# Performance work log

Measured on AMD Instinct MI355X. Metric: run time of the kernel, lower is better.

Reference implementation:

```python
import jax, jax.numpy as jnp
import numpy as np

B, C, F = 4, 3, 5
HO, WO = 256, 256
HI, WI = HO + F - 1, WO + F - 1


def setup_inputs() -> dict:
    key = jax.random.key(0)
    k = jax.random.split(key, 6)
    return {
        "tensorInput": jax.random.normal(k[0], (B, C, HI, WI), dtype=jnp.float32),
        "tensorVertical": jax.random.uniform(k[1], (B, F, HO, WO), dtype=jnp.float32),
        "tensorHorizontal": jax.random.uniform(k[2], (B, F, HO, WO), dtype=jnp.float32),
        "tensorOffsetX": jax.random.normal(k[3], (B, F * F, HO, WO), dtype=jnp.float32),
        "tensorOffsetY": jax.random.normal(k[4], (B, F * F, HO, WO), dtype=jnp.float32),
        "tensorMask": jax.random.uniform(k[5], (B, F * F, HO, WO), dtype=jnp.float32),
    }


def _dsepconv(inp, vertical, horizontal, offset_x, offset_y, mask):
    b, c, hin, win = inp.shape
    f = vertical.shape[1]
    ho, wo = vertical.shape[2], vertical.shape[3]
    half = (f - 1) / 2.0

    fy = jnp.arange(f, dtype=inp.dtype).reshape(f, 1, 1, 1)
    fx = jnp.arange(f, dtype=inp.dtype).reshape(1, f, 1, 1)
    hg = jnp.arange(ho, dtype=inp.dtype).reshape(1, 1, ho, 1)
    wg = jnp.arange(wo, dtype=inp.dtype).reshape(1, 1, 1, wo)

    off_y = offset_y.reshape(b, f, f, ho, wo)  # note: code uses offset_y for delta_x
    off_x = offset_x.reshape(b, f, f, ho, wo)  # and offset_x for delta_y

    # sample positions per tap, [B,F,F,Ho,Wo]
    px = jnp.clip(off_y + wg + fx - half + 1.0, 0.0, win - 1)
    py = jnp.clip(off_x + hg + fy - half + 1.0, 0.0, hin - 1)

    left_f = jnp.floor(px)
    top_f = jnp.floor(py)
    wx = 1.0 - (px - left_f)  # bilinear weights
    wy = 1.0 - (py - top_f)

    l = left_f.astype(jnp.int32)
    t = top_f.astype(jnp.int32)
    r = jnp.minimum(l + 1, win - 1)
    btm = jnp.minimum(t + 1, hin - 1)

    def gather(img, yi, xi):
        return img[:, yi, xi]

    g = jax.vmap(gather)
    v_tl = g(inp, t, l)
    v_tr = g(inp, t, r)
    v_bl = g(inp, btm, l)
    v_br = g(inp, btm, r)

    wx_ = wx[:, None]  # add channel axis -> [B,1,F,F,Ho,Wo]
    wy_ = wy[:, None]
    val = (v_tl * wx_ * wy_ + v_tr * (1 - wx_) * wy_
           + v_bl * wx_ * (1 - wy_) + v_br * (1 - wx_) * (1 - wy_))

    # separable filter x mask per tap: [B,F,F,Ho,Wo]
    w_tap = vertical[:, :, None] * horizontal[:, None, :] * mask.reshape(b, f, f, ho, wo)
    # accumulate over the F*F taps
    return jnp.sum(val * w_tap[:, None], axis=(2, 3))  # [B,C,Ho,Wo]


def reference(tensorInput, tensorVertical, tensorHorizontal, tensorOffsetX, tensorOffsetY, tensorMask):
    return _dsepconv(tensorInput, tensorVertical, tensorHorizontal,
                     tensorOffsetX, tensorOffsetY, tensorMask)
```

## Files before the change

kernel.cpp:

```cpp
#include <hip/hip_runtime.h>
#include <hip/hip_fp16.h>

constexpr int B  = 4;
constexpr int C  = 3;
constexpr int F  = 5;
constexpr int HO = 256;
constexpr int WO = 256;
constexpr int HI = HO + F - 1;
constexpr int WI = WO + F - 1;
constexpr int P  = HO * WO;
constexpr int FF = F * F;
constexpr int PI = HI * WI;

constexpr int TROWS = 18;
constexpr int TCOLS = 80;
constexpr int TSTRIDE = 81;
constexpr int TN = TROWS * TCOLS;
constexpr int AMAX = (TROWS - 2) * TSTRIDE + (TCOLS - 2);

__device__ __forceinline__ uint2 pack3(float a, float b, float c) {
    __half2 ab = __floats2half2_rn(a, b);
    __half2 cz = __floats2half2_rn(c, 0.0f);
    uint2 r;
    r.x = *reinterpret_cast<const unsigned int*>(&ab);
    r.y = *reinterpret_cast<const unsigned int*>(&cz);
    return r;
}

__device__ __forceinline__ void fmacc(uint2 v, float w,
                                      float& a0, float& a1, float& a2) {
    __half2 ab = *reinterpret_cast<const __half2*>(&v.x);
    __half2 cz = *reinterpret_cast<const __half2*>(&v.y);
    a0 += __half2float(__low2half(ab))  * w;
    a1 += __half2float(__high2half(ab)) * w;
    a2 += __half2float(__low2half(cz))  * w;
}

__global__ __launch_bounds__(320, 8) void dsepconv_kernel(
    const float* __restrict__ inp,
    const float* __restrict__ vert,
    const float* __restrict__ horz,
    const float* __restrict__ offX,
    const float* __restrict__ offY,
    const float* __restrict__ mask,
    float* __restrict__ out)
{
    __shared__ uint2 tileq[TROWS * TSTRIDE];

    const int tid  = threadIdx.x;
    const int lane = tid & 63;
    const int wave = tid >> 6;

    const int idx0 = blockIdx.x * 64;
    const int idx  = idx0 + lane;
    const int x    = idx & (WO - 1);
    const int y    = (idx >> 8) & (HO - 1);
    const int b    = idx >> 16;
    const int x0   = idx0 & (WO - 1);
    const int pix  = y * WO + x;

    const float* in0 = inp + (size_t)b * C * PI;
    const float* in1 = in0 + PI;
    const float* in2 = in1 + PI;

    const int ry0 = y - 7;
    const int cx0 = x0 - 7;
#pragma unroll 1
    for (int e = tid; e < TN; e += 320) {
        int trow = e / TCOLS;
        int tcol = e - trow * TCOLS;
        int gy = min(max(ry0 + trow, 0), HI - 1);
        int gx = min(max(cx0 + tcol, 0), WI - 1);
        int g = gy * WI + gx;
        tileq[trow * TSTRIDE + tcol] = pack3(in0[g], in1[g], in2[g]);
    }
    __syncthreads();

    const float* offXb = offX + (size_t)b * FF * P + pix;
    const float* offYb = offY + (size_t)b * FF * P + pix;
    const float* maskb = mask + (size_t)b * FF * P + pix;
    const float* vb    = vert + (size_t)b * F * P + pix;
    const float* hb    = horz + (size_t)b * F * P + pix;

    const int i = wave;
    const float v = vb[i * P];
    const float py_base = (float)(y + i - 1);

    float acc0 = 0.f, acc1 = 0.f, acc2 = 0.f;

#pragma unroll 1
    for (int j = 0; j < F; ++j) {
        const int k = i * F + j;

        float oy = offYb[k * P];
        float ox = offXb[k * P];
        float m  = maskb[k * P];
        float h  = hb[j * P];

        float px = fminf(fmaxf(oy + (float)(x + j - 1), 0.0f), (float)(WI - 1));
        float py = fminf(fmaxf(ox + py_base, 0.0f), (float)(HI - 1));

        float lf = floorf(px);
        float tf = floorf(py);
        int l = (int)lf;
        int t = (int)tf;
        float wx = 1.0f - (px - lf);
        float wy = 1.0f - (py - tf);

        float w   = v * h * m;
        float wyw = wy * w;
        float wbw = w - wyw;
        float wtl = wx * wyw;
        float wtr = wyw - wtl;
        float wbl = wx * wbw;
        float wbr = wbw - wbl;

        int lt = t - ry0;
        int ll = l - cx0;
        bool ok = ((unsigned)lt <= TROWS - 2) & ((unsigned)ll <= TCOLS - 2);

        int a = min(max(lt * TSTRIDE + ll, 0), AMAX);

        uint2 g_tl = tileq[a];
        uint2 g_tr = tileq[a + 1];
        uint2 g_bl = tileq[a + TSTRIDE];
        uint2 g_br = tileq[a + TSTRIDE + 1];

        if (__any(!ok)) {
            if (!ok) {
                int r  = min(l + 1, WI - 1);
                int bt = min(t + 1, HI - 1);
                int o_tl = t * WI + l,  o_tr = t * WI + r;
                int o_bl = bt * WI + l, o_br = bt * WI + r;
                g_tl = pack3(in0[o_tl], in1[o_tl], in2[o_tl]);
                g_tr = pack3(in0[o_tr], in1[o_tr], in2[o_tr]);
                g_bl = pack3(in0[o_bl], in1[o_bl], in2[o_bl]);
                g_br = pack3(in0[o_br], in1[o_br], in2[o_br]);
            }
        }

        fmacc(g_tl, wtl, acc0, acc1, acc2);
        fmacc(g_tr, wtr, acc0, acc1, acc2);
        fmacc(g_bl, wbl, acc0, acc1, acc2);
        fmacc(g_br, wbr, acc0, acc1, acc2);
    }

    __syncthreads();
    float* red = (float*)tileq;
    red[(wave * 3 + 0) * 64 + lane] = acc0;
    red[(wave * 3 + 1) * 64 + lane] = acc1;
    red[(wave * 3 + 2) * 64 + lane] = acc2;
    __syncthreads();

    if (tid < 192) {
        const int ch = tid >> 6;
        const int ln = tid & 63;
        float s = red[(0 * 3 + ch) * 64 + ln]
                + red[(1 * 3 + ch) * 64 + ln]
                + red[(2 * 3 + ch) * 64 + ln]
                + red[(3 * 3 + ch) * 64 + ln]
                + red[(4 * 3 + ch) * 64 + ln];
        const int sidx = idx0 + ln;
        const int sb   = sidx >> 16;
        const int spix = sidx & (P - 1);
        out[(size_t)sb * C * P + (size_t)ch * P + spix] = s;
    }
}

extern "C" void kernel_launch(void* const* d_in, const int* in_sizes, int n_in,
                              void* d_out, int out_size, void* d_ws, size_t ws_size,
                              hipStream_t stream) {
    const float* inp  = (const float*)d_in[0];
    const float* vert = (const float*)d_in[1];
    const float* horz = (const float*)d_in[2];
    const float* offX = (const float*)d_in[3];
    const float* offY = (const float*)d_in[4];
    const float* mask = (const float*)d_in[5];
    float* out = (float*)d_out;

    const int total = B * HO * WO;
    dim3 block(320);
    dim3 grid(total / 64);
    dsepconv_kernel<<<grid, block, 0, stream>>>(inp, vert, horz, offX, offY, mask, out);
}
```

Baseline: 27.03 us.

## Tile 4 output rows per block and drop cross-wave tap reduction

Each block now computes a 4x64 output tile with one wave per row, each wave looping over all 25 taps. A 21-row shared tile serves four output rows instead of an 18-row tile per single row, cutting redundant input staging. The shared-memory reduction across waves and its barriers are removed, and results are written directly. In exchange there are fewer blocks and a longer serial per-thread loop, which may reduce latency hiding.

New measurement: 28.85 us. 6.8% more time.

```diff
diff --git a/kernel.cpp b/kernel.cpp
--- a/kernel.cpp
+++ b/kernel.cpp
@@ -12,7 +12,7 @@
 constexpr int FF = F * F;
 constexpr int PI = HI * WI;
 
-constexpr int TROWS = 18;
+constexpr int TROWS = 21;
 constexpr int TCOLS = 80;
 constexpr int TSTRIDE = 81;
 constexpr int TN = TROWS * TCOLS;
@@ -36,7 +36,7 @@
     a2 += __half2float(__low2half(cz))  * w;
 }
 
-__global__ __launch_bounds__(320, 8) void dsepconv_kernel(
+__global__ __launch_bounds__(256, 4) void dsepconv_kernel(
     const float* __restrict__ inp,
     const float* __restrict__ vert,
     const float* __restrict__ horz,
@@ -51,22 +51,19 @@
     const int lane = tid & 63;
     const int wave = tid >> 6;
 
-    const int idx0 = blockIdx.x * 64;
-    const int idx  = idx0 + lane;
-    const int x    = idx & (WO - 1);
-    const int y    = (idx >> 8) & (HO - 1);
-    const int b    = idx >> 16;
-    const int x0   = idx0 & (WO - 1);
-    const int pix  = y * WO + x;
+    const int bx   = blockIdx.x;
+    const int x0   = (bx & 3) * 64;
+    const int y0   = ((bx >> 2) & 63) * 4;
+    const int b    = bx >> 8;
 
     const float* in0 = inp + (size_t)b * C * PI;
     const float* in1 = in0 + PI;
     const float* in2 = in1 + PI;
 
-    const int ry0 = y - 7;
+    const int ry0 = y0 - 7;
     const int cx0 = x0 - 7;
 #pragma unroll 1
-    for (int e = tid; e < TN; e += 320) {
+    for (int e = tid; e < TN; e += 256) {
         int trow = e / TCOLS;
         int tcol = e - trow * TCOLS;
         int gy = min(max(ry0 + trow, 0), HI - 1);
@@ -76,95 +73,85 @@
     }
     __syncthreads();
 
+    const int x   = x0 + lane;
+    const int y   = y0 + wave;
+    const int pix = y * WO + x;
+
     const float* offXb = offX + (size_t)b * FF * P + pix;
     const float* offYb = offY + (size_t)b * FF * P + pix;
     const float* maskb = mask + (size_t)b * FF * P + pix;
     const float* vb    = vert + (size_t)b * F * P + pix;
     const float* hb    = horz + (size_t)b * F * P + pix;
 
-    const int i = wave;
-    const float v = vb[i * P];
-    const float py_base = (float)(y + i - 1);
-
     float acc0 = 0.f, acc1 = 0.f, acc2 = 0.f;
 
 #pragma unroll 1
-    for (int j = 0; j < F; ++j) {
-        const int k = i * F + j;
+    for (int i = 0; i < F; ++i) {
+        const float v = vb[i * P];
+        const float py_base = (float)(y + i - 1);
 
-        float oy = offYb[k * P];
-        float ox = offXb[k * P];
-        float m  = maskb[k * P];
-        float h  = hb[j * P];
+#pragma unroll 1
+        for (int j = 0; j < F; ++j) {
+            const int k = i * F + j;
 
-        float px = fminf(fmaxf(oy + (float)(x + j - 1), 0.0f), (float)(WI - 1));
-        float py = fminf(fmaxf(ox + py_base, 0.0f), (float)(HI - 1));
+            float oy = offYb[k * P];
+            float ox = offXb[k * P];
+            float m  = maskb[k * P];
+            float h  = hb[j * P];
 
-        float lf = floorf(px);
-        float tf = floorf(py);
-        int l = (int)lf;
-        int t = (int)tf;
-        float wx = 1.0f - (px - lf);
-        float wy = 1.0f - (py - tf);
+            float px = fminf(fmaxf(oy + (float)(x + j - 1), 0.0f), (float)(WI - 1));
+            float py = fminf(fmaxf(ox + py_base, 0.0f), (float)(HI - 1));
 
-        float w   = v * h * m;
-        float wyw = wy * w;
-        float wbw = w - wyw;
-        float wtl = wx * wyw;
-        float wtr = wyw - wtl;
-        float wbl = wx * wbw;
-        float wbr = wbw - wbl;
+            float lf = floorf(px);
+            float tf = floorf(py);
+            int l = (int)lf;
+            int t = (int)tf;
+            float wx = 1.0f - (px - lf);
+            float wy = 1.0f - (py - tf);
 
-        int lt = t - ry0;
-        int ll = l - cx0;
-        bool ok = ((unsigned)lt <= TROWS - 2) & ((unsigned)ll <= TCOLS - 2);
+            float w   = v * h * m;
+            float wyw = wy * w;
+            float wbw = w - wyw;
+            float wtl = wx * wyw;
+            float wtr = wyw - wtl;
+            float wbl = wx * wbw;
+            float wbr = wbw - wbl;
 
-        int a = min(max(lt * TSTRIDE + ll, 0), AMAX);
+            int lt = t - ry0;
+            int ll = l - cx0;
+            bool ok = ((unsigned)lt <= TROWS - 2) & ((unsigned)ll <= TCOLS - 2);
 
-        uint2 g_tl = tileq[a];
-        uint2 g_tr = tileq[a + 1];
-        uint2 g_bl = tileq[a + TSTRIDE];
-        uint2 g_br = tileq[a + TSTRIDE + 1];
+            int a = min(max(lt * TSTRIDE + ll, 0), AMAX);
 
-        if (__any(!ok)) {
-            if (!ok) {
-                int r  = min(l + 1, WI - 1);
-                int bt = min(t + 1, HI - 1);
-                int o_tl = t * WI + l,  o_tr = t * WI + r;
-                int o_bl = bt * WI + l, o_br = bt * WI + r;
-                g_tl = pack3(in0[o_tl], in1[o_tl], in2[o_tl]);
-                g_tr = pack3(in0[o_tr], in1[o_tr], in2[o_tr]);
-                g_bl = pack3(in0[o_bl], in1[o_bl], in2[o_bl]);
-                g_br = pack3(in0[o_br], in1[o_br], in2[o_br]);
+            uint2 g_tl = tileq[a];
+            uint2 g_tr = tileq[a + 1];
+            uint2 g_bl = tileq[a + TSTRIDE];
+            uint2 g_br = tileq[a + TSTRIDE + 1];
+
+            if (__any(!ok)) {
+                if (!ok) {
+                    int r  = min(l + 1, WI - 1);
+                    int bt = min(t + 1, HI - 1);
+                    int o_tl = t * WI + l,  o_tr = t * WI + r;
+                    int o_bl = bt * WI + l, o_br = bt * WI + r;
+                    g_tl = pack3(in0[o_tl], in1[o_tl], in2[o_tl]);
+                    g_tr = pack3(in0[o_tr], in1[o_tr], in2[o_tr]);
+                    g_bl = pack3(in0[o_bl], in1[o_bl], in2[o_bl]);
+                    g_br = pack3(in0[o_br], in1[o_br], in2[o_br]);
+                }
             }
+
+            fmacc(g_tl, wtl, acc0, acc1, acc2);
+            fmacc(g_tr, wtr, acc0, acc1, acc2);
+            fmacc(g_bl, wbl, acc0, acc1, acc2);
+            fmacc(g_br, wbr, acc0, acc1, acc2);
         }
-
-        fmacc(g_tl, wtl, acc0, acc1, acc2);
-        fmacc(g_tr, wtr, acc0, acc1, acc2);
-        fmacc(g_bl, wbl, acc0, acc1, acc2);
-        fmacc(g_br, wbr, acc0, acc1, acc2);
     }
 
-    __syncthreads();
-    float* red = (float*)tileq;
-    red[(wave * 3 + 0) * 64 + lane] = acc0;
-    red[(wave * 3 + 1) * 64 + lane] = acc1;
-    red[(wave * 3 + 2) * 64 + lane] = acc2;
-    __syncthreads();
-
-    if (tid < 192) {
-        const int ch = tid >> 6;
-        const int ln = tid & 63;
-        float s = red[(0 * 3 + ch) * 64 + ln]
-                + red[(1 * 3 + ch) * 64 + ln]
-                + red[(2 * 3 + ch) * 64 + ln]
-                + red[(3 * 3 + ch) * 64 + ln]
-                + red[(4 * 3 + ch) * 64 + ln];
-        const int sidx = idx0 + ln;
-        const int sb   = sidx >> 16;
-        const int spix = sidx & (P - 1);
-        out[(size_t)sb * C * P + (size_t)ch * P + spix] = s;
-    }
+    float* ob = out + (size_t)b * C * P + pix;
+    ob[0]     = acc0;
+    ob[P]     = acc1;
+    ob[2 * P] = acc2;
 }
 
 extern "C" void kernel_launch(void* const* d_in, const int* in_sizes, int n_in,
@@ -178,8 +165,7 @@
     const float* mask = (const float*)d_in[5];
     float* out = (float*)d_out;
 
-    const int total = B * HO * WO;
-    dim3 block(320);
-    dim3 grid(total / 64);
+    dim3 block(256);
+    dim3 grid(B * (HO / 4) * (WO / 64));
     dsepconv_kernel<<<grid, block, 0, stream>>>(inp, vert, horz, offX, offY, mask, out);
 }
```
